# Kernel tuning notes

Hardware: AMD Instinct MI355X
Metric: run time of the kernel (lower is better)

The kernel has to match this reference:

```python
import jax, jax.numpy as jnp
import numpy as np

N_NODES = 50000
N_EDGES = 1_600_000
NODE_DIM = 64
EDGE_DIM = 2
F_HID = 64            # node_hidden
E_HID = 16            # edge_hidden
EGO_HID = F_HID // 2  # 32
PEER_HID = F_HID - EGO_HID  # 32
HDIM = F_HID + 3 * E_HID    # 112
BN_EPS = 1e-5


def _linear_params(key, fan_in, fan_out):
    # torch.nn.Linear default init: U(-1/sqrt(fan_in), 1/sqrt(fan_in))
    lim = 1.0 / np.sqrt(fan_in)
    kw, kb = jax.random.split(key)
    W = jax.random.uniform(kw, (fan_in, fan_out), minval=-lim, maxval=lim, dtype=jnp.float32)
    b = jax.random.uniform(kb, (fan_out,), minval=-lim, maxval=lim, dtype=jnp.float32)
    return W, b


def setup_inputs() -> dict:
    key = jax.random.key(0)
    ks = jax.random.split(key, 12)
    x = jax.random.normal(ks[0], (N_NODES, NODE_DIM), dtype=jnp.float32)
    edge_attrs = jax.random.uniform(ks[1], (N_EDGES, EDGE_DIM), dtype=jnp.float32)
    treatments = jax.random.uniform(ks[2], (N_NODES,), dtype=jnp.float32)
    src = jax.random.randint(ks[3], (N_EDGES,), 0, N_NODES)
    dst = jax.random.randint(ks[4], (N_EDGES,), 0, N_NODES)

    W_peer, b_peer = _linear_params(ks[5], NODE_DIM + EDGE_DIM, PEER_HID + E_HID)
    W_ego, b_ego = _linear_params(ks[6], NODE_DIM, EGO_HID)
    W_edge, b_edge = _linear_params(ks[7], EDGE_DIM, E_HID)
    W_emb, b_emb = _linear_params(ks[8], HDIM, F_HID)
    W0, b0 = _linear_params(ks[9], F_HID, 1)
    W1, b1 = _linear_params(ks[10], F_HID, 1)

    bn_gamma = jnp.ones((F_HID,), jnp.float32)
    bn_beta = jnp.zeros((F_HID,), jnp.float32)
    bn_mean = jnp.zeros((F_HID,), jnp.float32)
    bn_var = jnp.ones((F_HID,), jnp.float32)

    return dict(x=x, edge_attrs=edge_attrs, treatments=treatments, src=src, dst=dst,
                W_peer=W_peer, b_peer=b_peer, W_ego=W_ego, b_ego=b_ego,
                W_edge=W_edge, b_edge=b_edge, W_emb=W_emb, b_emb=b_emb,
                bn_gamma=bn_gamma, bn_beta=bn_beta, bn_mean=bn_mean, bn_var=bn_var,
                W0=W0, b0=b0, W1=W1, b1=b1)


def _forward(x, edge_attrs, treatments, src, dst,
             W_peer, b_peer, W_ego, b_ego, W_edge, b_edge,
             W_emb, b_emb, bn_gamma, bn_beta, bn_mean, bn_var, W0, b0, W1, b1):
    n = x.shape[0]
    seg = lambda v, idx: jax.ops.segment_sum(v, idx, num_segments=n)

    # ---- CANE feature embedding (edge-list gather -> MLP -> scatter-sum) ----
    # degree-normalization: deg = adj_t.sum(1) (in-degree at dst), deg^-0.5, inf->0
    deg = seg(jnp.ones((src.shape[0],), x.dtype), dst)  # [N]
    deg_inv = jnp.where(deg > 0, deg ** -0.5, 0.0)

    h_ego = jax.nn.relu(x @ W_ego + b_ego)  # [N, EGO_HID]

    # per-edge peer MLP, normalized scatter to dst
    peer_feat = jnp.concatenate([x[dst], edge_attrs], axis=1)        # [E, NODE_DIM+EDGE_DIM]
    peer_msg = (peer_feat @ W_peer + b_peer) * deg_inv[dst][:, None]  # [E, PEER_HID+E_HID]
    h_peer = jax.nn.relu(seg(peer_msg, dst))                          # [N, PEER_HID+E_HID]

    # per-edge edge MLP, scatter to dst; plus degree-normalized 2-hop aggregate
    h_e = jax.nn.relu(edge_attrs @ W_edge + b_edge)                   # [E, E_HID]
    h_edge_agg = seg(h_e, dst)                                        # [N, E_HID]
    h_edge_2hop = seg(deg_inv[dst][:, None] * h_edge_agg[src], dst)   # [N, E_HID]

    f_emb = jnp.concatenate([h_ego, h_edge_agg, h_edge_2hop, h_peer], axis=1)  # [N, HDIM]
    f_emb = jax.nn.relu(f_emb)

    # ---- TLearner dense heads ----
    emb = jax.nn.relu(f_emb @ W_emb + b_emb)                          # [N, F_HID]
    emb = (emb - bn_mean) * jax.lax.rsqrt(bn_var + BN_EPS) * bn_gamma + bn_beta
    emb = jnp.tanh(emb)
    y0_pred = (emb @ W0 + b0).reshape(-1)
    y1_pred = (emb @ W1 + b1).reshape(-1)
    return y0_pred, y1_pred, emb


def reference(x, edge_attrs, treatments, src, dst,
              W_peer, b_peer, W_ego, b_ego, W_edge, b_edge,
              W_emb, b_emb, bn_gamma, bn_beta, bn_mean, bn_var, W0, b0, W1, b1):
    return _forward(x, edge_attrs, treatments, src, dst,
                    W_peer, b_peer, W_ego, b_ego, W_edge, b_edge,
                    W_emb, b_emb, bn_gamma, bn_beta, bn_mean, bn_var, W0, b0, W1, b1)
```

## Files before the change

kernel.cpp:

```cpp
#include <hip/hip_runtime.h>
#include <math.h>



__global__ void k_countR(const int* __restrict__ dst, int* __restrict__ counts,
                         int* __restrict__ rank, int nE) {
    int e = blockIdx.x * blockDim.x + threadIdx.x;
    if (e < nE) rank[e] = atomicAdd(&counts[dst[e]], 1);
}

__global__ void k_count(const int* __restrict__ dst, int* __restrict__ counts,
                        int nE) {
    int e = blockIdx.x * blockDim.x + threadIdx.x;
    if (e < nE) atomicAdd(&counts[dst[e]], 1);
}

template <bool WRITE_CURSOR>
__global__ __launch_bounds__(1024) void k_scan(const int* __restrict__ counts,
                                               int* __restrict__ rowstart,
                                               int* __restrict__ cursor,
                                               int nN, int nE) {
    __shared__ int s[1024];
    int t = threadIdx.x;
    int C = (nN + 1023) / 1024;
    int lo = min(t * C, nN), hi = min(lo + C, nN);
    int sum = 0;
    for (int i = lo; i < hi; ++i) sum += counts[i];
    s[t] = sum;
    __syncthreads();
    for (int off = 1; off < 1024; off <<= 1) {
        int v = (t >= off) ? s[t - off] : 0;
        __syncthreads();
        s[t] += v;
        __syncthreads();
    }
    int run = (t == 0) ? 0 : s[t - 1];
    for (int i = lo; i < hi; ++i) {
        rowstart[i] = run;
        if (WRITE_CURSOR) cursor[i] = run;
        run += counts[i];
    }
    if (t == 0) rowstart[nN] = nE;
}


__global__ void k_fillR(const int* __restrict__ dst, const int* __restrict__ src,
                        const float* __restrict__ ea, const int* __restrict__ rank,
                        const int* __restrict__ rowstart,
                        int4* __restrict__ payload, int nE) {
    int e = blockIdx.x * blockDim.x + threadIdx.x;
    if (e < nE) {
        float2 eav = ((const float2*)ea)[e];
        int d = dst[e];
        int slot = rowstart[d] + rank[e];
        int4 p;
        p.x = __float_as_int(eav.x);
        p.y = __float_as_int(eav.y);
        p.z = src[e];
        p.w = 0;
        payload[slot] = p;
    }
}

__global__ void k_fillP(const int* __restrict__ dst, const int* __restrict__ src,
                        const float* __restrict__ ea, int* __restrict__ cursor,
                        int4* __restrict__ payload, int nE) {
    int e = blockIdx.x * blockDim.x + threadIdx.x;
    if (e < nE) {
        float2 eav = ((const float2*)ea)[e];
        int sn = src[e];
        int slot = atomicAdd(&cursor[dst[e]], 1);
        int4 p;
        p.x = __float_as_int(eav.x);
        p.y = __float_as_int(eav.y);
        p.z = sn;
        p.w = 0;
        payload[slot] = p;
    }
}


__global__ void k_aggP1(const int4* __restrict__ payload,
                        const int* __restrict__ rowstart,
                        const float* __restrict__ We, const float* __restrict__ be,
                        float* __restrict__ eagg, float* __restrict__ easum,
                        int nN) {
    __shared__ float w[48];
    if (threadIdx.x < 32) w[threadIdx.x] = We[threadIdx.x];
    else if (threadIdx.x < 48) w[threadIdx.x] = be[threadIdx.x - 32];
    __syncthreads();
    int gid = blockIdx.x * blockDim.x + threadIdx.x;
    int v = gid >> 4, j = gid & 15;
    if (v >= nN) return;
    int s0 = rowstart[v], s1 = rowstart[v + 1];
    float acc = 0.f, aE = 0.f;
    for (int s = s0; s < s1; ++s) {
        int4 p = payload[s];
        float ea0 = __int_as_float(p.x), ea1 = __int_as_float(p.y);
        acc += fmaxf(fmaf(ea0, w[j], fmaf(ea1, w[16 + j], w[32 + j])), 0.f);
        if (j == 0) aE += ea0;
        else if (j == 1) aE += ea1;
    }
    eagg[v * 16 + j] = acc;
    if (j == 0) easum[2 * v] = aE;
    else if (j == 1) easum[2 * v + 1] = aE;
}

__global__ void k_aggP2(const int4* __restrict__ payload,
                        const int* __restrict__ rowstart,
                        const float* __restrict__ eagg, float* __restrict__ h2,
                        int nN) {
    int gid = blockIdx.x * blockDim.x + threadIdx.x;
    int v = gid >> 4, j = gid & 15;
    if (v >= nN) return;
    int s0 = rowstart[v], s1 = rowstart[v + 1];
    float acc = 0.f;
    for (int s = s0; s < s1; ++s) {
        int sn = payload[s].z;
        acc += eagg[sn * 16 + j];
    }
    h2[v * 16 + j] = acc;
}


__global__ void k_edge1(const float* __restrict__ ea, const int* __restrict__ dst,
                        const float* __restrict__ We, const float* __restrict__ be,
                        float* __restrict__ deg, float* __restrict__ easum,
                        float* __restrict__ eagg, int nE) {
    __shared__ float w[48];
    if (threadIdx.x < 32) w[threadIdx.x] = We[threadIdx.x];
    else if (threadIdx.x < 48) w[threadIdx.x] = be[threadIdx.x - 32];
    __syncthreads();
    const float2* ea2 = (const float2*)ea;
    long long stride = (long long)gridDim.x * blockDim.x;
    for (long long gid = (long long)blockIdx.x * blockDim.x + threadIdx.x;
         gid < 16LL * nE; gid += stride) {
        int e = (int)(gid >> 4);
        int j = (int)(gid & 15);
        int d = dst[e];
        float2 eav = ea2[e];
        float h = fmaxf(fmaf(eav.x, w[j], fmaf(eav.y, w[16 + j], w[32 + j])), 0.f);
        atomicAdd(&eagg[d * 16 + j], h);
        if (j == 0)      atomicAdd(&deg[d], 1.0f);
        else if (j == 1) atomicAdd(&easum[2 * d], eav.x);
        else if (j == 2) atomicAdd(&easum[2 * d + 1], eav.y);
    }
}

__global__ void k_edge2(const int* __restrict__ src, const int* __restrict__ dst,
                        const float* __restrict__ eagg, float* __restrict__ h2,
                        int nE) {
    long long stride = (long long)gridDim.x * blockDim.x;
    for (long long gid = (long long)blockIdx.x * blockDim.x + threadIdx.x;
         gid < 16LL * nE; gid += stride) {
        int e = (int)(gid >> 4);
        int j = (int)(gid & 15);
        atomicAdd(&h2[dst[e] * 16 + j], eagg[src[e] * 16 + j]);
    }
}


template <bool DEG_FROM_CSR>
__global__ __launch_bounds__(256) void k_nodeA(
    const float* __restrict__ x,
    const float* __restrict__ W_ego, const float* __restrict__ b_ego,
    const float* __restrict__ W_peer, const float* __restrict__ b_peer,
    const float* __restrict__ degf, const int* __restrict__ rowstart,
    const float* __restrict__ easum,
    const float* __restrict__ eagg, const float* __restrict__ h2,
    float* __restrict__ femb, int nN) {
    __shared__ __align__(16) float sWe[64 * 32];
    __shared__ __align__(16) float sWp[64 * 48];
    __shared__ float sWpe[96];
    __shared__ float sbe[32];
    __shared__ float sbp[48];
    for (int i = threadIdx.x; i < 64 * 32; i += 256) sWe[i] = W_ego[i];
    for (int i = threadIdx.x; i < 64 * 48; i += 256) sWp[i] = W_peer[i];
    if (threadIdx.x < 96) sWpe[threadIdx.x] = W_peer[64 * 48 + threadIdx.x];
    if (threadIdx.x < 32) sbe[threadIdx.x] = b_ego[threadIdx.x];
    if (threadIdx.x < 48) sbp[threadIdx.x] = b_peer[threadIdx.x];
    __syncthreads();

    int v = blockIdx.x * 256 + threadIdx.x;
    if (v >= nN) return;

    float accE[32];
    float accP[48];
#pragma unroll
    for (int j = 0; j < 32; ++j) accE[j] = 0.f;
#pragma unroll
    for (int j = 0; j < 48; ++j) accP[j] = 0.f;

    const float4* x4 = (const float4*)(x + (long long)v * 64);
#pragma unroll 4
    for (int k4 = 0; k4 < 16; ++k4) {
        float4 xv = x4[k4];
        float xs[4] = {xv.x, xv.y, xv.z, xv.w};
#pragma unroll
        for (int t = 0; t < 4; ++t) {
            int k = 4 * k4 + t;
            float xk = xs[t];
            const float4* we4 = (const float4*)&sWe[k * 32];
#pragma unroll
            for (int j4 = 0; j4 < 8; ++j4) {
                float4 w = we4[j4];
                accE[4 * j4 + 0] = fmaf(xk, w.x, accE[4 * j4 + 0]);
                accE[4 * j4 + 1] = fmaf(xk, w.y, accE[4 * j4 + 1]);
                accE[4 * j4 + 2] = fmaf(xk, w.z, accE[4 * j4 + 2]);
                accE[4 * j4 + 3] = fmaf(xk, w.w, accE[4 * j4 + 3]);
            }
            const float4* wp4 = (const float4*)&sWp[k * 48];
#pragma unroll
            for (int j4 = 0; j4 < 12; ++j4) {
                float4 w = wp4[j4];
                accP[4 * j4 + 0] = fmaf(xk, w.x, accP[4 * j4 + 0]);
                accP[4 * j4 + 1] = fmaf(xk, w.y, accP[4 * j4 + 1]);
                accP[4 * j4 + 2] = fmaf(xk, w.z, accP[4 * j4 + 2]);
                accP[4 * j4 + 3] = fmaf(xk, w.w, accP[4 * j4 + 3]);
            }
        }
    }

    float dg;
    if (DEG_FROM_CSR) dg = (float)(rowstart[v + 1] - rowstart[v]);
    else              dg = degf[v];
    float dinv = dg > 0.f ? 1.0f / sqrtf(dg) : 0.f;
    float ea0 = easum[2 * v], ea1 = easum[2 * v + 1];

    float* fo = femb + (long long)v * 112;
#pragma unroll
    for (int j = 0; j < 32; ++j) fo[j] = fmaxf(accE[j] + sbe[j], 0.f);
#pragma unroll
    for (int j = 0; j < 16; ++j) fo[32 + j] = eagg[v * 16 + j];
#pragma unroll
    for (int j = 0; j < 16; ++j) fo[48 + j] = dinv * h2[v * 16 + j];
#pragma unroll
    for (int j = 0; j < 48; ++j) {
        float t = dg * (accP[j] + sbp[j]) + fmaf(ea0, sWpe[j], ea1 * sWpe[48 + j]);
        fo[64 + j] = fmaxf(dinv * t, 0.f);
    }
}

__global__ __launch_bounds__(256) void k_nodeB(
    const float* __restrict__ femb,
    const float* __restrict__ W_emb, const float* __restrict__ b_emb,
    const float* __restrict__ bn_g, const float* __restrict__ bn_b,
    const float* __restrict__ bn_m, const float* __restrict__ bn_v,
    const float* __restrict__ W0, const float* __restrict__ b0,
    const float* __restrict__ W1, const float* __restrict__ b1,
    float* __restrict__ out, int nN) {
    __shared__ __align__(16) float sW[112 * 64];
    __shared__ float sbias[64], sScale[64], sShift[64], sW0[64], sW1[64];
    for (int i = threadIdx.x; i < 112 * 64; i += 256) sW[i] = W_emb[i];
    if (threadIdx.x < 64) {
        int j = threadIdx.x;
        sbias[j] = b_emb[j];
        float rstd = 1.0f / sqrtf(bn_v[j] + 1e-5f);
        float sc = bn_g[j] * rstd;
        sScale[j] = sc;
        sShift[j] = bn_b[j] - bn_m[j] * sc;
        sW0[j] = W0[j];
        sW1[j] = W1[j];
    }
    __syncthreads();

    int v = blockIdx.x * 256 + threadIdx.x;
    if (v >= nN) return;

    float acc[64];
#pragma unroll
    for (int j = 0; j < 64; ++j) acc[j] = 0.f;

    const float4* f4 = (const float4*)(femb + (long long)v * 112);
#pragma unroll 4
    for (int k4 = 0; k4 < 28; ++k4) {
        float4 fv = f4[k4];
        float fs[4] = {fv.x, fv.y, fv.z, fv.w};
#pragma unroll
        for (int t = 0; t < 4; ++t) {
            int k = 4 * k4 + t;
            float fk = fs[t];
            const float4* wr4 = (const float4*)&sW[k * 64];
#pragma unroll
            for (int j4 = 0; j4 < 16; ++j4) {
                float4 w = wr4[j4];
                acc[4 * j4 + 0] = fmaf(fk, w.x, acc[4 * j4 + 0]);
                acc[4 * j4 + 1] = fmaf(fk, w.y, acc[4 * j4 + 1]);
                acc[4 * j4 + 2] = fmaf(fk, w.z, acc[4 * j4 + 2]);
                acc[4 * j4 + 3] = fmaf(fk, w.w, acc[4 * j4 + 3]);
            }
        }
    }

    float y0 = 0.f, y1 = 0.f;
#pragma unroll
    for (int j = 0; j < 64; ++j) {
        float e = fmaxf(acc[j] + sbias[j], 0.f);
        e = fmaf(e, sScale[j], sShift[j]);
        e = tanhf(e);
        acc[j] = e;
        y0 = fmaf(e, sW0[j], y0);
        y1 = fmaf(e, sW1[j], y1);
    }

    float4* o4 = (float4*)(out + 2LL * nN + (long long)v * 64);
#pragma unroll
    for (int j4 = 0; j4 < 16; ++j4)
        o4[j4] = make_float4(acc[4 * j4], acc[4 * j4 + 1], acc[4 * j4 + 2], acc[4 * j4 + 3]);
    out[v] = y0 + b0[0];
    out[nN + v] = y1 + b1[0];
}


extern "C" void kernel_launch(void* const* d_in, const int* in_sizes, int n_in,
                              void* d_out, int out_size, void* d_ws, size_t ws_size,
                              hipStream_t stream) {
    const float* x      = (const float*)d_in[0];
    const float* ea     = (const float*)d_in[1];
    const int*   src    = (const int*)d_in[3];
    const int*   dst    = (const int*)d_in[4];
    const float* W_peer = (const float*)d_in[5];
    const float* b_peer = (const float*)d_in[6];
    const float* W_ego  = (const float*)d_in[7];
    const float* b_ego  = (const float*)d_in[8];
    const float* W_edge = (const float*)d_in[9];
    const float* b_edge = (const float*)d_in[10];
    const float* W_emb  = (const float*)d_in[11];
    const float* b_emb  = (const float*)d_in[12];
    const float* bn_g   = (const float*)d_in[13];
    const float* bn_b   = (const float*)d_in[14];
    const float* bn_m   = (const float*)d_in[15];
    const float* bn_v   = (const float*)d_in[16];
    const float* W0     = (const float*)d_in[17];
    const float* b0     = (const float*)d_in[18];
    const float* W1     = (const float*)d_in[19];
    const float* b1     = (const float*)d_in[20];

    int nE = in_sizes[3];
    int nN = in_sizes[2];

    int nBlocks  = (nN + 255) / 256;
    int ngBlocks = (16 * nN + 255) / 256;
    int eBlocks1 = (nE + 255) / 256;

    size_t fixed1   = (size_t)36 * nN + 4;
    size_t fixed1Al = (fixed1 + 3) & ~(size_t)3;
    size_t regElems = 5ULL * nE + 4;
    size_t fembEl   = (size_t)112 * nN;
    size_t t1El     = fixed1Al + (regElems > fembEl ? regElems : fembEl);
    size_t fixed2   = (size_t)37 * nN + 4;
    size_t fixed2Al = (fixed2 + 3) & ~(size_t)3;
    size_t reg2     = 4ULL * nE + 4;
    size_t t2El     = fixed2Al + (reg2 > fembEl ? reg2 : fembEl);

    if (ws_size >= 4 * t1El) {
        int*   wsi      = (int*)d_ws;
        int*   counts   = wsi;
        int*   rowstart = wsi + nN;
        float* eagg     = (float*)(wsi + 2 * nN + 4);
        float* easum    = eagg + 16LL * nN;
        float* h2       = easum + 2LL * nN;
        int*   rank     = wsi + fixed1Al;
        size_t payOff   = (fixed1Al + (size_t)nE + 3) & ~(size_t)3;
        int4*  payload  = (int4*)(wsi + payOff);
        float* femb     = (float*)(wsi + fixed1Al);

        hipMemsetAsync(counts, 0, sizeof(int) * (size_t)nN, stream);
        k_countR<<<eBlocks1, 256, 0, stream>>>(dst, counts, rank, nE);
        k_scan<false><<<1, 1024, 0, stream>>>(counts, rowstart, nullptr, nN, nE);
        k_fillR<<<eBlocks1, 256, 0, stream>>>(dst, src, ea, rank, rowstart,
                                              payload, nE);
        k_aggP1<<<ngBlocks, 256, 0, stream>>>(payload, rowstart, W_edge, b_edge,
                                              eagg, easum, nN);
        k_aggP2<<<ngBlocks, 256, 0, stream>>>(payload, rowstart, eagg, h2, nN);
        k_nodeA<true><<<nBlocks, 256, 0, stream>>>(x, W_ego, b_ego, W_peer, b_peer,
                                                   nullptr, rowstart, easum,
                                                   eagg, h2, femb, nN);
        k_nodeB<<<nBlocks, 256, 0, stream>>>(femb, W_emb, b_emb, bn_g, bn_b, bn_m,
                                             bn_v, W0, b0, W1, b1, (float*)d_out, nN);
    } else if (ws_size >= 4 * t2El) {
        int*   wsi      = (int*)d_ws;
        int*   counts   = wsi;
        int*   rowstart = wsi + nN;
        int*   cursor   = wsi + 2 * nN + 4;
        float* eagg     = (float*)(wsi + 3 * nN + 4);
        float* easum    = eagg + 16LL * nN;
        float* h2       = easum + 2LL * nN;
        int4*  payload  = (int4*)(wsi + fixed2Al);
        float* femb     = (float*)(wsi + fixed2Al);

        hipMemsetAsync(counts, 0, sizeof(int) * (size_t)nN, stream);
        k_count<<<eBlocks1, 256, 0, stream>>>(dst, counts, nE);
        k_scan<true><<<1, 1024, 0, stream>>>(counts, rowstart, cursor, nN, nE);
        k_fillP<<<eBlocks1, 256, 0, stream>>>(dst, src, ea, cursor, payload, nE);
        k_aggP1<<<ngBlocks, 256, 0, stream>>>(payload, rowstart, W_edge, b_edge,
                                              eagg, easum, nN);
        k_aggP2<<<ngBlocks, 256, 0, stream>>>(payload, rowstart, eagg, h2, nN);
        k_nodeA<true><<<nBlocks, 256, 0, stream>>>(x, W_ego, b_ego, W_peer, b_peer,
                                                   nullptr, rowstart, easum,
                                                   eagg, h2, femb, nN);
        k_nodeB<<<nBlocks, 256, 0, stream>>>(femb, W_emb, b_emb, bn_g, bn_b, bn_m,
                                             bn_v, W0, b0, W1, b1, (float*)d_out, nN);
    } else {
        float* wsf   = (float*)d_ws;
        float* deg   = wsf;
        float* easum = wsf + nN;
        float* eagg  = wsf + 3LL * nN;
        float* h2    = wsf + 19LL * nN;
        float* femb  = wsf + 35LL * nN;

        hipMemsetAsync(wsf, 0, sizeof(float) * 35ULL * nN, stream);
        const int eBlocks = 2048;
        k_edge1<<<eBlocks, 256, 0, stream>>>(ea, dst, W_edge, b_edge, deg, easum,
                                             eagg, nE);
        k_edge2<<<eBlocks, 256, 0, stream>>>(src, dst, eagg, h2, nE);
        k_nodeA<false><<<nBlocks, 256, 0, stream>>>(x, W_ego, b_ego, W_peer, b_peer,
                                                    deg, nullptr, easum,
                                                    eagg, h2, femb, nN);
        k_nodeB<<<nBlocks, 256, 0, stream>>>(femb, W_emb, b_emb, bn_g, bn_b, bn_m,
                                             bn_v, W0, b0, W1, b1, (float*)d_out, nN);
    }
}
```

Baseline: 428.0 us.

## Split node dense layers across 8 threads per node with shared-memory staged inputs

Rewrites the two node-level dense kernels so that each node is handled by a group of 8 threads, with each thread computing a slice of output columns. The node rows (x or femb) for 32 nodes are staged into shared memory with coalesced float4 loads, and the head outputs are reduced with warp shuffles. This cuts per-thread register pressure (80 or 64 accumulators down to 10 or 8) and replaces strided per-thread row reads with coalesced ones, aiming for higher occupancy and better memory efficiency. In exchange the grid is 8x larger and the weight matrix is reloaded into shared memory by 8x more blocks.

```diff
diff --git a/kernel.cpp b/kernel.cpp
--- a/kernel.cpp
+++ b/kernel.cpp
@@ -171,6 +171,7 @@
     float* __restrict__ femb, int nN) {
     __shared__ __align__(16) float sWe[64 * 32];
     __shared__ __align__(16) float sWp[64 * 48];
+    __shared__ __align__(16) float sx[32 * 64];
     __shared__ float sWpe[96];
     __shared__ float sbe[32];
     __shared__ float sbp[48];
@@ -179,46 +180,47 @@
     if (threadIdx.x < 96) sWpe[threadIdx.x] = W_peer[64 * 48 + threadIdx.x];
     if (threadIdx.x < 32) sbe[threadIdx.x] = b_ego[threadIdx.x];
     if (threadIdx.x < 48) sbp[threadIdx.x] = b_peer[threadIdx.x];
+
+    long long base = (long long)blockIdx.x * 32;
+    {
+        int nv = (int)min(32LL, (long long)nN - base);
+        if (nv > 0) {
+            const float4* xs = (const float4*)(x + base * 64);
+            int lim = nv * 16;
+            for (int i = threadIdx.x; i < lim; i += 256)
+                ((float4*)sx)[i] = xs[i];
+        }
+    }
     __syncthreads();
 
-    int v = blockIdx.x * 256 + threadIdx.x;
+    int g = threadIdx.x >> 3;
+    int t = threadIdx.x & 7;
+    long long v = base + g;
     if (v >= nN) return;
 
-    float accE[32];
-    float accP[48];
-#pragma unroll
-    for (int j = 0; j < 32; ++j) accE[j] = 0.f;
-#pragma unroll
-    for (int j = 0; j < 48; ++j) accP[j] = 0.f;
-
-    const float4* x4 = (const float4*)(x + (long long)v * 64);
-#pragma unroll 4
-    for (int k4 = 0; k4 < 16; ++k4) {
-        float4 xv = x4[k4];
-        float xs[4] = {xv.x, xv.y, xv.z, xv.w};
-#pragma unroll
-        for (int t = 0; t < 4; ++t) {
-            int k = 4 * k4 + t;
-            float xk = xs[t];
-            const float4* we4 = (const float4*)&sWe[k * 32];
-#pragma unroll
-            for (int j4 = 0; j4 < 8; ++j4) {
-                float4 w = we4[j4];
-                accE[4 * j4 + 0] = fmaf(xk, w.x, accE[4 * j4 + 0]);
-                accE[4 * j4 + 1] = fmaf(xk, w.y, accE[4 * j4 + 1]);
-                accE[4 * j4 + 2] = fmaf(xk, w.z, accE[4 * j4 + 2]);
-                accE[4 * j4 + 3] = fmaf(xk, w.w, accE[4 * j4 + 3]);
-            }
-            const float4* wp4 = (const float4*)&sWp[k * 48];
-#pragma unroll
-            for (int j4 = 0; j4 < 12; ++j4) {
-                float4 w = wp4[j4];
-                accP[4 * j4 + 0] = fmaf(xk, w.x, accP[4 * j4 + 0]);
-                accP[4 * j4 + 1] = fmaf(xk, w.y, accP[4 * j4 + 1]);
-                accP[4 * j4 + 2] = fmaf(xk, w.z, accP[4 * j4 + 2]);
-                accP[4 * j4 + 3] = fmaf(xk, w.w, accP[4 * j4 + 3]);
-            }
-        }
+    float accE[4] = {0.f, 0.f, 0.f, 0.f};
+    float accP[6] = {0.f, 0.f, 0.f, 0.f, 0.f, 0.f};
+    const float* xv = &sx[g * 64];
+    const float4* sWe4 = (const float4*)sWe;
+    const float2* sWp2 = (const float2*)sWp;
+
+#pragma unroll 8
+    for (int k = 0; k < 64; ++k) {
+        float xk = xv[k];
+        float4 we = sWe4[k * 8 + t];
+        accE[0] = fmaf(xk, we.x, accE[0]);
+        accE[1] = fmaf(xk, we.y, accE[1]);
+        accE[2] = fmaf(xk, we.z, accE[2]);
+        accE[3] = fmaf(xk, we.w, accE[3]);
+        float2 w0 = sWp2[k * 24 + t * 3];
+        float2 w1 = sWp2[k * 24 + t * 3 + 1];
+        float2 w2 = sWp2[k * 24 + t * 3 + 2];
+        accP[0] = fmaf(xk, w0.x, accP[0]);
+        accP[1] = fmaf(xk, w0.y, accP[1]);
+        accP[2] = fmaf(xk, w1.x, accP[2]);
+        accP[3] = fmaf(xk, w1.y, accP[3]);
+        accP[4] = fmaf(xk, w2.x, accP[4]);
+        accP[5] = fmaf(xk, w2.y, accP[5]);
     }
 
     float dg;
@@ -227,17 +229,29 @@
     float dinv = dg > 0.f ? 1.0f / sqrtf(dg) : 0.f;
     float ea0 = easum[2 * v], ea1 = easum[2 * v + 1];
 
-    float* fo = femb + (long long)v * 112;
+    float* fo = femb + v * 112;
+    {
+        float4 e;
+        e.x = fmaxf(accE[0] + sbe[4 * t + 0], 0.f);
+        e.y = fmaxf(accE[1] + sbe[4 * t + 1], 0.f);
+        e.z = fmaxf(accE[2] + sbe[4 * t + 2], 0.f);
+        e.w = fmaxf(accE[3] + sbe[4 * t + 3], 0.f);
+        ((float4*)fo)[t] = e;
+    }
+    if (t < 4) {
+        float4 gv = ((const float4*)(eagg + v * 16))[t];
+        ((float4*)fo)[8 + t] = gv;
+    } else {
+        int tt = t - 4;
+        float4 hv = ((const float4*)(h2 + v * 16))[tt];
+        hv.x *= dinv; hv.y *= dinv; hv.z *= dinv; hv.w *= dinv;
+        ((float4*)fo)[12 + tt] = hv;
+    }
 #pragma unroll
-    for (int j = 0; j < 32; ++j) fo[j] = fmaxf(accE[j] + sbe[j], 0.f);
-#pragma unroll
-    for (int j = 0; j < 16; ++j) fo[32 + j] = eagg[v * 16 + j];
-#pragma unroll
-    for (int j = 0; j < 16; ++j) fo[48 + j] = dinv * h2[v * 16 + j];
-#pragma unroll
-    for (int j = 0; j < 48; ++j) {
-        float t = dg * (accP[j] + sbp[j]) + fmaf(ea0, sWpe[j], ea1 * sWpe[48 + j]);
-        fo[64 + j] = fmaxf(dinv * t, 0.f);
+    for (int i = 0; i < 6; ++i) {
+        int c = 6 * t + i;
+        float tv = dg * (accP[i] + sbp[c]) + fmaf(ea0, sWpe[c], ea1 * sWpe[48 + c]);
+        fo[64 + c] = fmaxf(dinv * tv, 0.f);
     }
 }
 
@@ -250,8 +264,10 @@
     const float* __restrict__ W1, const float* __restrict__ b1,
     float* __restrict__ out, int nN) {
     __shared__ __align__(16) float sW[112 * 64];
+    __shared__ __align__(16) float sf[32 * 112];
     __shared__ float sbias[64], sScale[64], sShift[64], sW0[64], sW1[64];
-    for (int i = threadIdx.x; i < 112 * 64; i += 256) sW[i] = W_emb[i];
+    for (int i = threadIdx.x; i < 112 * 16; i += 256)
+        ((float4*)sW)[i] = ((const float4*)W_emb)[i];
     if (threadIdx.x < 64) {
         int j = threadIdx.x;
         sbias[j] = b_emb[j];
@@ -262,53 +278,69 @@
         sW0[j] = W0[j];
         sW1[j] = W1[j];
     }
+    long long base = (long long)blockIdx.x * 32;
+    {
+        int nv = (int)min(32LL, (long long)nN - base);
+        if (nv > 0) {
+            const float4* fs = (const float4*)(femb + base * 112);
+            int lim = nv * 28;
+            for (int i = threadIdx.x; i < lim; i += 256)
+                ((float4*)sf)[i] = fs[i];
+        }
+    }
     __syncthreads();
 
-    int v = blockIdx.x * 256 + threadIdx.x;
+    int g = threadIdx.x >> 3;
+    int t = threadIdx.x & 7;
+    long long v = base + g;
     if (v >= nN) return;
 
-    float acc[64];
+    float acc[8];
 #pragma unroll
-    for (int j = 0; j < 64; ++j) acc[j] = 0.f;
-
-    const float4* f4 = (const float4*)(femb + (long long)v * 112);
-#pragma unroll 4
-    for (int k4 = 0; k4 < 28; ++k4) {
-        float4 fv = f4[k4];
-        float fs[4] = {fv.x, fv.y, fv.z, fv.w};
-#pragma unroll
-        for (int t = 0; t < 4; ++t) {
-            int k = 4 * k4 + t;
-            float fk = fs[t];
-            const float4* wr4 = (const float4*)&sW[k * 64];
-#pragma unroll
-            for (int j4 = 0; j4 < 16; ++j4) {
-                float4 w = wr4[j4];
-                acc[4 * j4 + 0] = fmaf(fk, w.x, acc[4 * j4 + 0]);
-                acc[4 * j4 + 1] = fmaf(fk, w.y, acc[4 * j4 + 1]);
-                acc[4 * j4 + 2] = fmaf(fk, w.z, acc[4 * j4 + 2]);
-                acc[4 * j4 + 3] = fmaf(fk, w.w, acc[4 * j4 + 3]);
-            }
-        }
+    for (int j = 0; j < 8; ++j) acc[j] = 0.f;
+
+    const float* fv = &sf[g * 112];
+    const float4* sW4 = (const float4*)sW;
+
+#pragma unroll 8
+    for (int k = 0; k < 112; ++k) {
+        float f = fv[k];
+        float4 wa = sW4[k * 16 + t * 2];
+        float4 wb = sW4[k * 16 + t * 2 + 1];
+        acc[0] = fmaf(f, wa.x, acc[0]);
+        acc[1] = fmaf(f, wa.y, acc[1]);
+        acc[2] = fmaf(f, wa.z, acc[2]);
+        acc[3] = fmaf(f, wa.w, acc[3]);
+        acc[4] = fmaf(f, wb.x, acc[4]);
+        acc[5] = fmaf(f, wb.y, acc[5]);
+        acc[6] = fmaf(f, wb.z, acc[6]);
+        acc[7] = fmaf(f, wb.w, acc[7]);
     }
 
     float y0 = 0.f, y1 = 0.f;
 #pragma unroll
-    for (int j = 0; j < 64; ++j) {
-        float e = fmaxf(acc[j] + sbias[j], 0.f);
-        e = fmaf(e, sScale[j], sShift[j]);
+    for (int j = 0; j < 8; ++j) {
+        int c = 8 * t + j;
+        float e = fmaxf(acc[j] + sbias[c], 0.f);
+        e = fmaf(e, sScale[c], sShift[c]);
         e = tanhf(e);
         acc[j] = e;
-        y0 = fmaf(e, sW0[j], y0);
-        y1 = fmaf(e, sW1[j], y1);
-    }
-
-    float4* o4 = (float4*)(out + 2LL * nN + (long long)v * 64);
+        y0 = fmaf(e, sW0[c], y0);
+        y1 = fmaf(e, sW1[c], y1);
+    }
 #pragma unroll
-    for (int j4 = 0; j4 < 16; ++j4)
-        o4[j4] = make_float4(acc[4 * j4], acc[4 * j4 + 1], acc[4 * j4 + 2], acc[4 * j4 + 3]);
-    out[v] = y0 + b0[0];
-    out[nN + v] = y1 + b1[0];
+    for (int off = 1; off < 8; off <<= 1) {
+        y0 += __shfl_xor(y0, off);
+        y1 += __shfl_xor(y1, off);
+    }
+
+    float4* o4 = (float4*)(out + 2LL * nN + v * 64 + t * 8);
+    o4[0] = make_float4(acc[0], acc[1], acc[2], acc[3]);
+    o4[1] = make_float4(acc[4], acc[5], acc[6], acc[7]);
+    if (t == 0) {
+        out[v] = y0 + b0[0];
+        out[nN + v] = y1 + b1[0];
+    }
 }
 
 
@@ -339,7 +371,7 @@
     int nE = in_sizes[3];
     int nN = in_sizes[2];
 
-    int nBlocks  = (nN + 255) / 256;
+    int nABlocks = (nN + 31) / 32;
     int ngBlocks = (16 * nN + 255) / 256;
     int eBlocks1 = (nE + 255) / 256;
 
@@ -373,11 +405,11 @@
         k_aggP1<<<ngBlocks, 256, 0, stream>>>(payload, rowstart, W_edge, b_edge,
                                               eagg, easum, nN);
         k_aggP2<<<ngBlocks, 256, 0, stream>>>(payload, rowstart, eagg, h2, nN);
-        k_nodeA<true><<<nBlocks, 256, 0, stream>>>(x, W_ego, b_ego, W_peer, b_peer,
-                                                   nullptr, rowstart, easum,
-                                                   eagg, h2, femb, nN);
-        k_nodeB<<<nBlocks, 256, 0, stream>>>(femb, W_emb, b_emb, bn_g, bn_b, bn_m,
-                                             bn_v, W0, b0, W1, b1, (float*)d_out, nN);
+        k_nodeA<true><<<nABlocks, 256, 0, stream>>>(x, W_ego, b_ego, W_peer, b_peer,
+                                                    nullptr, rowstart, easum,
+                                                    eagg, h2, femb, nN);
+        k_nodeB<<<nABlocks, 256, 0, stream>>>(femb, W_emb, b_emb, bn_g, bn_b, bn_m,
+                                              bn_v, W0, b0, W1, b1, (float*)d_out, nN);
     } else if (ws_size >= 4 * t2El) {
         int*   wsi      = (int*)d_ws;
         int*   counts   = wsi;
@@ -396,11 +428,11 @@
         k_aggP1<<<ngBlocks, 256, 0, stream>>>(payload, rowstart, W_edge, b_edge,
                                               eagg, easum, nN);
         k_aggP2<<<ngBlocks, 256, 0, stream>>>(payload, rowstart, eagg, h2, nN);
-        k_nodeA<true><<<nBlocks, 256, 0, stream>>>(x, W_ego, b_ego, W_peer, b_peer,
-                                                   nullptr, rowstart, easum,
-                                                   eagg, h2, femb, nN);
-        k_nodeB<<<nBlocks, 256, 0, stream>>>(femb, W_emb, b_emb, bn_g, bn_b, bn_m,
-                                             bn_v, W0, b0, W1, b1, (float*)d_out, nN);
+        k_nodeA<true><<<nABlocks, 256, 0, stream>>>(x, W_ego, b_ego, W_peer, b_peer,
+                                                    nullptr, rowstart, easum,
+                                                    eagg, h2, femb, nN);
+        k_nodeB<<<nABlocks, 256, 0, stream>>>(femb, W_emb, b_emb, bn_g, bn_b, bn_m,
+                                              bn_v, W0, b0, W1, b1, (float*)d_out, nN);
     } else {
         float* wsf   = (float*)d_ws;
         float* deg   = wsf;
@@ -414,10 +446,10 @@
         k_edge1<<<eBlocks, 256, 0, stream>>>(ea, dst, W_edge, b_edge, deg, easum,
                                              eagg, nE);
         k_edge2<<<eBlocks, 256, 0, stream>>>(src, dst, eagg, h2, nE);
-        k_nodeA<false><<<nBlocks, 256, 0, stream>>>(x, W_ego, b_ego, W_peer, b_peer,
-                                                    deg, nullptr, easum,
-                                                    eagg, h2, femb, nN);
-        k_nodeB<<<nBlocks, 256, 0, stream>>>(femb, W_emb, b_emb, bn_g, bn_b, bn_m,
-                                             bn_v, W0, b0, W1, b1, (float*)d_out, nN);
-    }
-}
+        k_nodeA<false><<<nABlocks, 256, 0, stream>>>(x, W_ego, b_ego, W_peer, b_peer,
+                                                     deg, nullptr, easum,
+                                                     eagg, h2, femb, nN);
+        k_nodeB<<<nABlocks, 256, 0, stream>>>(femb, W_emb, b_emb, bn_g, bn_b, bn_m,
+                                              bn_v, W0, b0, W1, b1, (float*)d_out, nN);
+    }
+}
```

Result: faster. 415.3 us (-3.0%).
